# Kernel optimization log

Hardware: AMD Instinct MI355X
Metric: run time of the kernel (lower is better)

The kernel has to match this reference:

```python
import jax, jax.numpy as jnp
import numpy as np
import itertools


def _trilinear_interpn(vol, loc):
    """N-D linear interpolation of vol [*spatial, C] at locations loc [*spatial, N].
    Faithful to the torch module: floor/clamp corners, per-corner gather on the
    flattened volume, weights diff_loc1 = loc1 - loc, diff_loc0 = 1 - diff_loc1.
    """
    nb_dims = loc.shape[-1]
    spatial = vol.shape[:-1]
    C = vol.shape[-1]
    # row-major strides over spatial dims (k in the torch code)
    strides = np.cumprod((spatial[1:] + (1,))[::-1])[::-1]  # e.g. (H*W, W, 1) for 3D

    loc0 = jnp.floor(loc)
    max_loc = [d - 1 for d in spatial]
    loc0c = [jnp.clip(loc0[..., d], 0, max_loc[d]) for d in range(nb_dims)]
    loc1 = [jnp.clip(loc0c[d] + 1, 0, max_loc[d]) for d in range(nb_dims)]
    locs = [[f.astype(jnp.int32) for f in loc0c],
            [f.astype(jnp.int32) for f in loc1]]
    diff_loc1 = [loc1[d] - loc[..., d] for d in range(nb_dims)]
    diff_loc0 = [1.0 - d for d in diff_loc1]
    weights = [diff_loc1, diff_loc0]  # weights[0] pairs with loc0 corner, [1] with loc1

    vol_flat = vol.reshape(-1, C)
    interp = jnp.zeros(spatial + (C,), dtype=vol.dtype)
    for c in itertools.product([0, 1], repeat=nb_dims):
        subs = [locs[c[d]][d] for d in range(nb_dims)]
        idx = subs[0] * int(strides[0])
        for d in range(1, nb_dims):
            idx = idx + subs[d] * int(strides[d])
        vol_val = jnp.take(vol_flat, idx.reshape(-1), axis=0).reshape(spatial + (C,))
        wt = weights[c[0]][0]
        for d in range(1, nb_dims):
            wt = wt * weights[c[d]][d]
        interp = interp + wt[..., None] * vol_val
    return interp


def setup_inputs() -> dict:
    key = jax.random.key(0)
    k1, k2 = jax.random.split(key)
    D, H, W, C = 160, 192, 160, 4
    vol = jax.random.normal(k1, (D, H, W, C), dtype=jnp.float32)
    df = jax.random.normal(k2, (D, H, W, 3), dtype=jnp.float32)
    return {"vol": vol, "df": df}


def reference(vol, df):
    spatial = df.shape[:-1]
    nb_dims = len(spatial)
    # identity grid + displacement field -> absolute sample locations
    mesh = jnp.meshgrid(*[jnp.arange(d, dtype=jnp.float32) for d in spatial],
                        indexing="ij")
    loc = jnp.stack([mesh[d] + df[..., d] for d in range(nb_dims)], axis=-1)
    return _trilinear_interpn(vol, loc)
```

## Files before the change

kernel.cpp:

```cpp
#include <hip/hip_runtime.h>
#include <hip/hip_fp16.h>

#define D_ 160
#define H_ 192
#define W_ 160
constexpr int NV = D_ * H_ * W_;

typedef float        f32x4 __attribute__((ext_vector_type(4)));
typedef unsigned int u32x4 __attribute__((ext_vector_type(4)));

__global__ __launch_bounds__(256) void vol_to_half_kernel(
    const float4* __restrict__ vol, uint4* __restrict__ volh2)
{
    unsigned bid = blockIdx.x;
    unsigned nb  = (bid & 7u) * 1200u + (bid >> 3);
    int i = (int)(nb * 256u + threadIdx.x);
    if (i >= NV / 2) return;
    f32x4 a = __builtin_nontemporal_load((const f32x4*)(vol + 2 * i));
    f32x4 b = __builtin_nontemporal_load((const f32x4*)(vol + 2 * i + 1));
    __half2 a01 = __floats2half2_rn(a.x, a.y);
    __half2 a23 = __floats2half2_rn(a.z, a.w);
    __half2 b01 = __floats2half2_rn(b.x, b.y);
    __half2 b23 = __floats2half2_rn(b.z, b.w);
    uint4 p;
    p.x = *(unsigned int*)&a01;
    p.y = *(unsigned int*)&a23;
    p.z = *(unsigned int*)&b01;
    p.w = *(unsigned int*)&b23;
    volh2[i] = p;
}

__device__ inline float4 h4_to_f4(uint2 p) {
    __half2 ab = *(__half2*)&p.x;
    __half2 cd = *(__half2*)&p.y;
    float2 f0 = __half22float2(ab);
    float2 f1 = __half22float2(cd);
    return make_float4(f0.x, f0.y, f1.x, f1.y);
}

struct VoxSetup {
    int b00, b01, b10, b11;
    float wz0, wz1, wy0, wy1, wx0, wx1;
};

__device__ inline VoxSetup setup_voxel(int x, int y, int z,
                                       float dz, float dy, float dx)
{
    float lz = (float)z + dz;
    float ly = (float)y + dy;
    float lx = (float)x + dx;

    float z0f = fminf(fmaxf(floorf(lz), 0.f), (float)(D_ - 1));
    float y0f = fminf(fmaxf(floorf(ly), 0.f), (float)(H_ - 1));
    float x0f = fminf(fmaxf(floorf(lx), 0.f), (float)(W_ - 1));
    float z1f = fminf(z0f + 1.f, (float)(D_ - 1));
    float y1f = fminf(y0f + 1.f, (float)(H_ - 1));
    float x1f = fminf(x0f + 1.f, (float)(W_ - 1));

    VoxSetup s;
    s.wz0 = z1f - lz; s.wz1 = 1.f - s.wz0;
    s.wy0 = y1f - ly; s.wy1 = 1.f - s.wy0;

    int ix0 = (int)x0f;
    bool edge = ix0 >= W_ - 1;
    int a = edge ? W_ - 2 : ix0;
    float wx0 = x1f - lx;
    s.wx0 = edge ? 0.f : wx0;
    s.wx1 = 1.f - s.wx0;

    int iz0 = (int)z0f, iz1 = (int)z1f;
    int iy0 = (int)y0f, iy1 = (int)y1f;
    s.b00 = (iz0 * H_ + iy0) * W_ + a;
    s.b01 = (iz0 * H_ + iy1) * W_ + a;
    s.b10 = (iz1 * H_ + iy0) * W_ + a;
    s.b11 = (iz1 * H_ + iy1) * W_ + a;
    return s;
}

__device__ inline f32x4 reduce_voxel(const VoxSetup& s,
                                     u32x4 q00, u32x4 q01, u32x4 q10, u32x4 q11)
{
    uint2 l00, h00, l01, h01, l10, h10, l11, h11;
    l00.x = q00[0]; l00.y = q00[1]; h00.x = q00[2]; h00.y = q00[3];
    l01.x = q01[0]; l01.y = q01[1]; h01.x = q01[2]; h01.y = q01[3];
    l10.x = q10[0]; l10.y = q10[1]; h10.x = q10[2]; h10.y = q10[3];
    l11.x = q11[0]; l11.y = q11[1]; h11.x = q11[2]; h11.y = q11[3];

    float4 v000 = h4_to_f4(l00), v001 = h4_to_f4(h00);
    float4 v010 = h4_to_f4(l01), v011 = h4_to_f4(h01);
    float4 v100 = h4_to_f4(l10), v101 = h4_to_f4(h10);
    float4 v110 = h4_to_f4(l11), v111 = h4_to_f4(h11);

    float w000 = s.wz0 * s.wy0 * s.wx0;
    float w001 = s.wz0 * s.wy0 * s.wx1;
    float w010 = s.wz0 * s.wy1 * s.wx0;
    float w011 = s.wz0 * s.wy1 * s.wx1;
    float w100 = s.wz1 * s.wy0 * s.wx0;
    float w101 = s.wz1 * s.wy0 * s.wx1;
    float w110 = s.wz1 * s.wy1 * s.wx0;
    float w111 = s.wz1 * s.wy1 * s.wx1;

    f32x4 r;
    r.x = w000 * v000.x + w001 * v001.x + w010 * v010.x + w011 * v011.x
        + w100 * v100.x + w101 * v101.x + w110 * v110.x + w111 * v111.x;
    r.y = w000 * v000.y + w001 * v001.y + w010 * v010.y + w011 * v011.y
        + w100 * v100.y + w101 * v101.y + w110 * v110.y + w111 * v111.y;
    r.z = w000 * v000.z + w001 * v001.z + w010 * v010.z + w011 * v011.z
        + w100 * v100.z + w101 * v101.z + w110 * v110.z + w111 * v111.z;
    r.w = w000 * v000.w + w001 * v001.w + w010 * v010.w + w011 * v011.w
        + w100 * v100.w + w101 * v101.w + w110 * v110.w + w111 * v111.w;
    return r;
}

__global__ __launch_bounds__(256) void st_half_kernel(
    const uint2* __restrict__ volh,
    const float* __restrict__ df,
    float*       __restrict__ out)
{
    unsigned bid = blockIdx.x;
    unsigned nb  = (bid & 7u) * 1200u + (bid >> 3);
    int bx = (int)(nb % 5u);
    unsigned rest = nb / 5u;
    int by = (int)(rest % 48u);
    int bz = (int)(rest / 48u);

    int tid = threadIdx.x;
    int xA = bx * 32 + (tid & 15);
    int y  = by * 4  + ((tid >> 4) & 3);
    int z  = bz * 4  + (tid >> 6);

    int idxA = (z * H_ + y) * W_ + xA;
    int idxB = idxA + 16;

    const float* dfpA = df + 3 * (size_t)idxA;
    const float* dfpB = df + 3 * (size_t)idxB;
    float dzA = __builtin_nontemporal_load(dfpA + 0);
    float dyA = __builtin_nontemporal_load(dfpA + 1);
    float dxA = __builtin_nontemporal_load(dfpA + 2);
    float dzB = __builtin_nontemporal_load(dfpB + 0);
    float dyB = __builtin_nontemporal_load(dfpB + 1);
    float dxB = __builtin_nontemporal_load(dfpB + 2);

    VoxSetup sA = setup_voxel(xA,      y, z, dzA, dyA, dxA);
    VoxSetup sB = setup_voxel(xA + 16, y, z, dzB, dyB, dxB);

    u32x4 qA00, qA01, qA10, qA11, qB00, qB01, qB10, qB11;
    __builtin_memcpy(&qA00, volh + sA.b00, 16);
    __builtin_memcpy(&qA01, volh + sA.b01, 16);
    __builtin_memcpy(&qA10, volh + sA.b10, 16);
    __builtin_memcpy(&qA11, volh + sA.b11, 16);
    __builtin_memcpy(&qB00, volh + sB.b00, 16);
    __builtin_memcpy(&qB01, volh + sB.b01, 16);
    __builtin_memcpy(&qB10, volh + sB.b10, 16);
    __builtin_memcpy(&qB11, volh + sB.b11, 16);

    f32x4 rA = reduce_voxel(sA, qA00, qA01, qA10, qA11);
    __builtin_nontemporal_store(rA, (f32x4*)(out + 4 * (size_t)idxA));
    f32x4 rB = reduce_voxel(sB, qB00, qB01, qB10, qB11);
    __builtin_nontemporal_store(rB, (f32x4*)(out + 4 * (size_t)idxB));
}

__global__ __launch_bounds__(256) void st_f32_kernel(
    const float4* __restrict__ vol,
    const float*  __restrict__ df,
    float4*       __restrict__ out)
{
    int tid = threadIdx.x;
    int x = blockIdx.x * 16 + (tid & 15);
    int y = blockIdx.y * 4  + ((tid >> 4) & 3);
    int z = blockIdx.z * 4  + (tid >> 6);
    int idx = (z * H_ + y) * W_ + x;

    float dz = df[3 * idx + 0];
    float dy = df[3 * idx + 1];
    float dx = df[3 * idx + 2];
    float lz = (float)z + dz, ly = (float)y + dy, lx = (float)x + dx;

    float z0f = fminf(fmaxf(floorf(lz), 0.f), (float)(D_ - 1));
    float y0f = fminf(fmaxf(floorf(ly), 0.f), (float)(H_ - 1));
    float x0f = fminf(fmaxf(floorf(lx), 0.f), (float)(W_ - 1));
    float z1f = fminf(z0f + 1.f, (float)(D_ - 1));
    float y1f = fminf(y0f + 1.f, (float)(H_ - 1));
    float x1f = fminf(x0f + 1.f, (float)(W_ - 1));

    float wz0 = z1f - lz, wz1 = 1.f - wz0;
    float wy0 = y1f - ly, wy1 = 1.f - wy0;
    float wx0 = x1f - lx, wx1 = 1.f - wx0;

    int iz0 = (int)z0f, iz1 = (int)z1f;
    int iy0 = (int)y0f, iy1 = (int)y1f;
    int ix0 = (int)x0f, ix1 = (int)x1f;

    int b00 = (iz0 * H_ + iy0) * W_;
    int b01 = (iz0 * H_ + iy1) * W_;
    int b10 = (iz1 * H_ + iy0) * W_;
    int b11 = (iz1 * H_ + iy1) * W_;

    float4 v000 = vol[b00 + ix0];
    float4 v001 = vol[b00 + ix1];
    float4 v010 = vol[b01 + ix0];
    float4 v011 = vol[b01 + ix1];
    float4 v100 = vol[b10 + ix0];
    float4 v101 = vol[b10 + ix1];
    float4 v110 = vol[b11 + ix0];
    float4 v111 = vol[b11 + ix1];

    float w000 = wz0*wy0*wx0, w001 = wz0*wy0*wx1;
    float w010 = wz0*wy1*wx0, w011 = wz0*wy1*wx1;
    float w100 = wz1*wy0*wx0, w101 = wz1*wy0*wx1;
    float w110 = wz1*wy1*wx0, w111 = wz1*wy1*wx1;

    float4 r;
    r.x = w000*v000.x + w001*v001.x + w010*v010.x + w011*v011.x
        + w100*v100.x + w101*v101.x + w110*v110.x + w111*v111.x;
    r.y = w000*v000.y + w001*v001.y + w010*v010.y + w011*v011.y
        + w100*v100.y + w101*v101.y + w110*v110.y + w111*v111.y;
    r.z = w000*v000.z + w001*v001.z + w010*v010.z + w011*v011.z
        + w100*v100.z + w101*v101.z + w110*v110.z + w111*v111.z;
    r.w = w000*v000.w + w001*v001.w + w010*v010.w + w011*v011.w
        + w100*v100.w + w101*v101.w + w110*v110.w + w111*v111.w;

    out[idx] = r;
}

extern "C" void kernel_launch(void* const* d_in, const int* in_sizes, int n_in,
                              void* d_out, int out_size, void* d_ws, size_t ws_size,
                              hipStream_t stream) {
    const float4* vol = (const float4*)d_in[0];
    const float*  df  = (const float*)d_in[1];
    float4* out = (float4*)d_out;

    size_t need = (size_t)NV * 8;
    if (ws_size >= need) {
        int pairs = NV / 2;
        vol_to_half_kernel<<<pairs / 256, 256, 0, stream>>>(
            vol, (uint4*)d_ws);
        st_half_kernel<<<9600, 256, 0, stream>>>(
            (const uint2*)d_ws, df, (float*)out);
    } else {
        dim3 grid(W_ / 16, H_ / 4, D_ / 4);
        st_f32_kernel<<<grid, 256, 0, stream>>>(vol, df, out);
    }
}
```

Measured before the change: 211.5 us.

## Process full x-rows per thread with software-pipelined gathers

Each block now covers a whole 160-wide row strip, and each thread walks 10 x-chunks in a loop. Within the loop it prefetches the next displacement and issues the current gathers before reducing the previous voxel. The grid shrinks from 9600 to 1920 blocks, with the XCD-interleaved block mapping adjusted to match. The aim is more memory-level parallelism per thread and better locality along x, at the cost of fewer waves, higher register pressure and possible tail imbalance.

```diff
diff --git a/kernel.cpp b/kernel.cpp
--- a/kernel.cpp
+++ b/kernel.cpp
@@ -118,46 +118,55 @@
     float*       __restrict__ out)
 {
     unsigned bid = blockIdx.x;
-    unsigned nb  = (bid & 7u) * 1200u + (bid >> 3);
-    int bx = (int)(nb % 5u);
-    unsigned rest = nb / 5u;
-    int by = (int)(rest % 48u);
-    int bz = (int)(rest / 48u);
+    unsigned nb  = (bid & 7u) * 240u + (bid >> 3);
+    int by = (int)(nb % 48u);
+    int bz = (int)(nb / 48u);
 
     int tid = threadIdx.x;
-    int xA = bx * 32 + (tid & 15);
-    int y  = by * 4  + ((tid >> 4) & 3);
-    int z  = bz * 4  + (tid >> 6);
-
-    int idxA = (z * H_ + y) * W_ + xA;
-    int idxB = idxA + 16;
-
-    const float* dfpA = df + 3 * (size_t)idxA;
-    const float* dfpB = df + 3 * (size_t)idxB;
-    float dzA = __builtin_nontemporal_load(dfpA + 0);
-    float dyA = __builtin_nontemporal_load(dfpA + 1);
-    float dxA = __builtin_nontemporal_load(dfpA + 2);
-    float dzB = __builtin_nontemporal_load(dfpB + 0);
-    float dyB = __builtin_nontemporal_load(dfpB + 1);
-    float dxB = __builtin_nontemporal_load(dfpB + 2);
-
-    VoxSetup sA = setup_voxel(xA,      y, z, dzA, dyA, dxA);
-    VoxSetup sB = setup_voxel(xA + 16, y, z, dzB, dyB, dxB);
-
-    u32x4 qA00, qA01, qA10, qA11, qB00, qB01, qB10, qB11;
-    __builtin_memcpy(&qA00, volh + sA.b00, 16);
-    __builtin_memcpy(&qA01, volh + sA.b01, 16);
-    __builtin_memcpy(&qA10, volh + sA.b10, 16);
-    __builtin_memcpy(&qA11, volh + sA.b11, 16);
-    __builtin_memcpy(&qB00, volh + sB.b00, 16);
-    __builtin_memcpy(&qB01, volh + sB.b01, 16);
-    __builtin_memcpy(&qB10, volh + sB.b10, 16);
-    __builtin_memcpy(&qB11, volh + sB.b11, 16);
-
-    f32x4 rA = reduce_voxel(sA, qA00, qA01, qA10, qA11);
-    __builtin_nontemporal_store(rA, (f32x4*)(out + 4 * (size_t)idxA));
-    f32x4 rB = reduce_voxel(sB, qB00, qB01, qB10, qB11);
-    __builtin_nontemporal_store(rB, (f32x4*)(out + 4 * (size_t)idxB));
+    int lx  = tid & 15;
+    int y   = by * 4 + ((tid >> 4) & 3);
+    int z   = bz * 4 + (tid >> 6);
+    int rowbase = (z * H_ + y) * W_;
+
+    float dzC, dyC, dxC;
+    {
+        const float* p = df + 3 * (size_t)(rowbase + lx);
+        dzC = __builtin_nontemporal_load(p + 0);
+        dyC = __builtin_nontemporal_load(p + 1);
+        dxC = __builtin_nontemporal_load(p + 2);
+    }
+
+    VoxSetup sP;
+    u32x4 qp0, qp1, qp2, qp3;
+
+    #pragma unroll
+    for (int bx = 0; bx < 10; ++bx) {
+        float dzN = 0.f, dyN = 0.f, dxN = 0.f;
+        if (bx < 9) {
+            const float* p = df + 3 * (size_t)(rowbase + (bx + 1) * 16 + lx);
+            dzN = __builtin_nontemporal_load(p + 0);
+            dyN = __builtin_nontemporal_load(p + 1);
+            dxN = __builtin_nontemporal_load(p + 2);
+        }
+        VoxSetup sC = setup_voxel(bx * 16 + lx, y, z, dzC, dyC, dxC);
+        u32x4 qc0, qc1, qc2, qc3;
+        __builtin_memcpy(&qc0, volh + sC.b00, 16);
+        __builtin_memcpy(&qc1, volh + sC.b01, 16);
+        __builtin_memcpy(&qc2, volh + sC.b10, 16);
+        __builtin_memcpy(&qc3, volh + sC.b11, 16);
+        if (bx > 0) {
+            f32x4 r = reduce_voxel(sP, qp0, qp1, qp2, qp3);
+            __builtin_nontemporal_store(
+                r, (f32x4*)(out + 4 * (size_t)(rowbase + (bx - 1) * 16 + lx)));
+        }
+        sP = sC; qp0 = qc0; qp1 = qc1; qp2 = qc2; qp3 = qc3;
+        dzC = dzN; dyC = dyN; dxC = dxN;
+    }
+    {
+        f32x4 r = reduce_voxel(sP, qp0, qp1, qp2, qp3);
+        __builtin_nontemporal_store(
+            r, (f32x4*)(out + 4 * (size_t)(rowbase + 9 * 16 + lx)));
+    }
 }
 
 __global__ __launch_bounds__(256) void st_f32_kernel(
@@ -235,7 +244,7 @@
         int pairs = NV / 2;
         vol_to_half_kernel<<<pairs / 256, 256, 0, stream>>>(
             vol, (uint4*)d_ws);
-        st_half_kernel<<<9600, 256, 0, stream>>>(
+        st_half_kernel<<<1920, 256, 0, stream>>>(
             (const uint2*)d_ws, df, (float*)out);
     } else {
         dim3 grid(W_ / 16, H_ / 4, D_ / 4);
```

After: 222.4 us. +5.2%, slower.

## Stage haloed fp16 volume tile in LDS via global_load_lds for gathers

Applied to the files above, without the earlier changes.

Each block now covers a 16x4x8 voxel region and first copies a haloed 24x14x16 fp16 window of the volume into shared memory with async global-to-LDS loads. Corner gathers read from LDS when all eight corners fall inside the window and fall back to global loads otherwise. The aim is to replace scattered global gathers with reuse of a shared tile. In exchange each block adds a synchronization barrier, about 43KB of LDS that may limit occupancy, and redundant halo traffic, since displacements are standard normal and most samples stay within a few voxels.

```diff
diff --git a/kernel.cpp b/kernel.cpp
--- a/kernel.cpp
+++ b/kernel.cpp
@@ -5,6 +5,11 @@
 #define H_ 192
 #define W_ 160
 constexpr int NV = D_ * H_ * W_;
+
+#define WX 24
+#define WY 14
+#define WZ 16
+#define NSTAGE ((WX / 2) * WY * WZ / 64)
 
 typedef float        f32x4 __attribute__((ext_vector_type(4)));
 typedef unsigned int u32x4 __attribute__((ext_vector_type(4)));
@@ -39,7 +44,7 @@
 }
 
 struct VoxSetup {
-    int b00, b01, b10, b11;
+    int a, iy0, iy1, iz0, iz1;
     float wz0, wz1, wy0, wy1, wx0, wx1;
 };
 
@@ -63,17 +68,13 @@
 
     int ix0 = (int)x0f;
     bool edge = ix0 >= W_ - 1;
-    int a = edge ? W_ - 2 : ix0;
+    s.a = edge ? W_ - 2 : ix0;
     float wx0 = x1f - lx;
     s.wx0 = edge ? 0.f : wx0;
     s.wx1 = 1.f - s.wx0;
 
-    int iz0 = (int)z0f, iz1 = (int)z1f;
-    int iy0 = (int)y0f, iy1 = (int)y1f;
-    s.b00 = (iz0 * H_ + iy0) * W_ + a;
-    s.b01 = (iz0 * H_ + iy1) * W_ + a;
-    s.b10 = (iz1 * H_ + iy0) * W_ + a;
-    s.b11 = (iz1 * H_ + iy1) * W_ + a;
+    s.iz0 = (int)z0f; s.iz1 = (int)z1f;
+    s.iy0 = (int)y0f; s.iy1 = (int)y1f;
     return s;
 }
 
@@ -112,25 +113,42 @@
     return r;
 }
 
+__device__ inline u32x4 lds_pair(const uint2 (*t)[WY][WX], int zz, int yy, int xx)
+{
+    uint2 lo = t[zz][yy][xx];
+    uint2 hi = t[zz][yy][xx + 1];
+    u32x4 q; q[0] = lo.x; q[1] = lo.y; q[2] = hi.x; q[3] = hi.y;
+    return q;
+}
+
 __global__ __launch_bounds__(256) void st_half_kernel(
     const uint2* __restrict__ volh,
     const float* __restrict__ df,
     float*       __restrict__ out)
 {
+    __shared__ alignas(16) uint2 tile[WZ][WY][WX];
+
     unsigned bid = blockIdx.x;
     unsigned nb  = (bid & 7u) * 1200u + (bid >> 3);
-    int bx = (int)(nb % 5u);
-    unsigned rest = nb / 5u;
+    int bx = (int)(nb % 10u);
+    unsigned rest = nb / 10u;
     int by = (int)(rest % 48u);
     int bz = (int)(rest / 48u);
 
-    int tid = threadIdx.x;
-    int xA = bx * 32 + (tid & 15);
+    int x_lo = bx * 16 - 4; x_lo = x_lo < 0 ? 0 : (x_lo > W_ - WX ? W_ - WX : x_lo);
+    int y_lo = by * 4  - 4; y_lo = y_lo < 0 ? 0 : (y_lo > H_ - WY ? H_ - WY : y_lo);
+    int z_lo = bz * 8  - 4; z_lo = z_lo < 0 ? 0 : (z_lo > D_ - WZ ? D_ - WZ : z_lo);
+
+    int tid  = threadIdx.x;
+    int lane = tid & 63;
+    int wid  = tid >> 6;
+
+    int x  = bx * 16 + (tid & 15);
     int y  = by * 4  + ((tid >> 4) & 3);
-    int z  = bz * 4  + (tid >> 6);
-
-    int idxA = (z * H_ + y) * W_ + xA;
-    int idxB = idxA + 16;
+    int zA = bz * 8  + wid;
+
+    int idxA = (zA * H_ + y) * W_ + x;
+    int idxB = idxA + 4 * H_ * W_;
 
     const float* dfpA = df + 3 * (size_t)idxA;
     const float* dfpB = df + 3 * (size_t)idxB;
@@ -141,23 +159,72 @@
     float dyB = __builtin_nontemporal_load(dfpB + 1);
     float dxB = __builtin_nontemporal_load(dfpB + 2);
 
-    VoxSetup sA = setup_voxel(xA,      y, z, dzA, dyA, dxA);
-    VoxSetup sB = setup_voxel(xA + 16, y, z, dzB, dyB, dxB);
-
-    u32x4 qA00, qA01, qA10, qA11, qB00, qB01, qB10, qB11;
-    __builtin_memcpy(&qA00, volh + sA.b00, 16);
-    __builtin_memcpy(&qA01, volh + sA.b01, 16);
-    __builtin_memcpy(&qA10, volh + sA.b10, 16);
-    __builtin_memcpy(&qA11, volh + sA.b11, 16);
-    __builtin_memcpy(&qB00, volh + sB.b00, 16);
-    __builtin_memcpy(&qB01, volh + sB.b01, 16);
-    __builtin_memcpy(&qB10, volh + sB.b10, 16);
-    __builtin_memcpy(&qB11, volh + sB.b11, 16);
-
-    f32x4 rA = reduce_voxel(sA, qA00, qA01, qA10, qA11);
-    __builtin_nontemporal_store(rA, (f32x4*)(out + 4 * (size_t)idxA));
-    f32x4 rB = reduce_voxel(sB, qB00, qB01, qB10, qB11);
-    __builtin_nontemporal_store(rB, (f32x4*)(out + 4 * (size_t)idxB));
+    #pragma unroll
+    for (int c0 = 0; c0 < 11; ++c0) {
+        int c = c0 * 4 + wid;
+        if (c < NSTAGE) {
+            int le  = c * 64 + lane;
+            int cx  = le % (WX / 2);
+            int row = le / (WX / 2);
+            int yy  = row % WY;
+            int zz  = row / WY;
+            const uint2* gp = volh +
+                ((size_t)((z_lo + zz) * H_ + (y_lo + yy)) * W_ + x_lo + cx * 2);
+            __builtin_amdgcn_global_load_lds(
+                (__attribute__((address_space(1))) void*)gp,
+                (__attribute__((address_space(3))) void*)
+                    ((char*)&tile[0][0][0] + c * 1024),
+                16, 0, 0);
+        }
+    }
+
+    VoxSetup sA = setup_voxel(x, y, zA,     dzA, dyA, dxA);
+    VoxSetup sB = setup_voxel(x, y, zA + 4, dzB, dyB, dxB);
+
+    __syncthreads();
+
+    {
+        const VoxSetup& s = sA;
+        bool ok = s.a >= x_lo && s.a <= x_lo + WX - 2
+               && s.iy0 >= y_lo && s.iy1 <= y_lo + WY - 1
+               && s.iz0 >= z_lo && s.iz1 <= z_lo + WZ - 1;
+        u32x4 q00, q01, q10, q11;
+        if (ok) {
+            int xx = s.a - x_lo;
+            q00 = lds_pair(tile, s.iz0 - z_lo, s.iy0 - y_lo, xx);
+            q01 = lds_pair(tile, s.iz0 - z_lo, s.iy1 - y_lo, xx);
+            q10 = lds_pair(tile, s.iz1 - z_lo, s.iy0 - y_lo, xx);
+            q11 = lds_pair(tile, s.iz1 - z_lo, s.iy1 - y_lo, xx);
+        } else {
+            __builtin_memcpy(&q00, volh + ((s.iz0 * H_ + s.iy0) * W_ + s.a), 16);
+            __builtin_memcpy(&q01, volh + ((s.iz0 * H_ + s.iy1) * W_ + s.a), 16);
+            __builtin_memcpy(&q10, volh + ((s.iz1 * H_ + s.iy0) * W_ + s.a), 16);
+            __builtin_memcpy(&q11, volh + ((s.iz1 * H_ + s.iy1) * W_ + s.a), 16);
+        }
+        f32x4 r = reduce_voxel(s, q00, q01, q10, q11);
+        __builtin_nontemporal_store(r, (f32x4*)(out + 4 * (size_t)idxA));
+    }
+    {
+        const VoxSetup& s = sB;
+        bool ok = s.a >= x_lo && s.a <= x_lo + WX - 2
+               && s.iy0 >= y_lo && s.iy1 <= y_lo + WY - 1
+               && s.iz0 >= z_lo && s.iz1 <= z_lo + WZ - 1;
+        u32x4 q00, q01, q10, q11;
+        if (ok) {
+            int xx = s.a - x_lo;
+            q00 = lds_pair(tile, s.iz0 - z_lo, s.iy0 - y_lo, xx);
+            q01 = lds_pair(tile, s.iz0 - z_lo, s.iy1 - y_lo, xx);
+            q10 = lds_pair(tile, s.iz1 - z_lo, s.iy0 - y_lo, xx);
+            q11 = lds_pair(tile, s.iz1 - z_lo, s.iy1 - y_lo, xx);
+        } else {
+            __builtin_memcpy(&q00, volh + ((s.iz0 * H_ + s.iy0) * W_ + s.a), 16);
+            __builtin_memcpy(&q01, volh + ((s.iz0 * H_ + s.iy1) * W_ + s.a), 16);
+            __builtin_memcpy(&q10, volh + ((s.iz1 * H_ + s.iy0) * W_ + s.a), 16);
+            __builtin_memcpy(&q11, volh + ((s.iz1 * H_ + s.iy1) * W_ + s.a), 16);
+        }
+        f32x4 r = reduce_voxel(s, q00, q01, q10, q11);
+        __builtin_nontemporal_store(r, (f32x4*)(out + 4 * (size_t)idxB));
+    }
 }
 
 __global__ __launch_bounds__(256) void st_f32_kernel(
```

Measured after the change: 210.5 us. About the same (-0.5%).
